# Performance work log

Hardware: AMD Instinct MI355X
Metric: run time of the kernel (lower is better)

Reference implementation:

```python
import jax, jax.numpy as jnp
import numpy as np

D_MODEL = 2048
HEADS = 32
HEAD_DIM = 64   # D_MODEL // HEADS
STATE = 256
KCONV = 4
CHUNK = 64
EPS = 1e-5
CONV_DIM = D_MODEL + 2 * STATE          # 2560 (n_groups=1)
PROJ = D_MODEL + CONV_DIM + HEADS       # 4640 (z | xBC | dt)
BATCH, SEQ = 2, 2048


def rmsnorm(x, w, eps=EPS):
    return x * jax.lax.rsqrt(jnp.mean(x * x, axis=-1, keepdims=True) + eps) * w


def setup_inputs() -> dict:
    key = jax.random.key(0)
    ks = jax.random.split(key, 8)
    x = jax.random.normal(ks[0], (BATCH, SEQ, D_MODEL), jnp.float32)
    norm_w = jnp.ones((D_MODEL,), jnp.float32)
    w_in = jax.random.normal(ks[1], (D_MODEL, PROJ), jnp.float32) * 0.02
    conv_w = jax.random.normal(ks[2], (CONV_DIM, KCONV), jnp.float32) * 0.2
    conv_b = jnp.zeros((CONV_DIM,), jnp.float32)
    # HF-style dt init: softplus(dt_bias) uniform-log in [1e-3, 1e-1]
    dt0 = jnp.exp(jax.random.uniform(ks[3], (HEADS,)) * (np.log(0.1) - np.log(0.001)) + np.log(0.001))
    dt_bias = dt0 + jnp.log(-jnp.expm1(-dt0))
    A_log = jnp.log(jnp.arange(1, HEADS + 1, dtype=jnp.float32))
    D_skip = jnp.ones((HEADS,), jnp.float32)
    gnorm_w = jnp.ones((D_MODEL,), jnp.float32)
    w_out = jax.random.normal(ks[4], (D_MODEL, D_MODEL), jnp.float32) * 0.02
    wo_w = jax.random.normal(ks[5], (D_MODEL, D_MODEL), jnp.float32) * 0.02
    return {"x": x, "norm_w": norm_w, "w_in": w_in, "conv_w": conv_w, "conv_b": conv_b,
            "dt_bias": dt_bias, "A_log": A_log, "D_skip": D_skip, "gnorm_w": gnorm_w,
            "w_out": w_out, "wo_w": wo_w}


def reference(x, norm_w, w_in, conv_w, conv_b, dt_bias, A_log, D_skip, gnorm_w, w_out, wo_w):
    b, L, _ = x.shape
    nc = L // CHUNK
    # pre-RMSNorm
    xn = rmsnorm(x, norm_w)
    # in_proj and split: z | xBC | dt
    proj = xn @ w_in
    z = proj[..., :D_MODEL]
    xBC = proj[..., D_MODEL:D_MODEL + CONV_DIM]
    dt = proj[..., D_MODEL + CONV_DIM:]                      # [b,L,H]
    # causal depthwise conv1d (kernel 4) + SiLU
    xp = jnp.pad(xBC, ((0, 0), (KCONV - 1, 0), (0, 0)))
    conv = conv_b + sum(xp[:, k:k + L] * conv_w[:, k] for k in range(KCONV))
    conv = jax.nn.silu(conv)
    xs = conv[..., :D_MODEL].reshape(b, L, HEADS, HEAD_DIM)  # SSM input
    Bm = conv[..., D_MODEL:D_MODEL + STATE]                  # [b,L,N] (n_groups=1)
    Cm = conv[..., D_MODEL + STATE:]                         # [b,L,N]
    dt = jax.nn.softplus(dt + dt_bias)                       # [b,L,H], >0
    A = -jnp.exp(A_log)                                      # [H]
    # ---- Mamba2 chunked selective scan (chunk_size=64) ----
    def ck(a):
        return a.reshape(b, nc, CHUNK, *a.shape[2:])
    xs_c, dt_c, B_c, C_c = ck(xs), ck(dt), ck(Bm), ck(Cm)
    Adt = dt_c * A                                           # [b,c,l,h] (<=0)
    Acs = jnp.cumsum(Adt, axis=2)
    # intra-chunk (diagonal blocks)
    seg = Acs[:, :, :, None, :] - Acs[:, :, None, :, :]      # [b,c,l,s,h]
    idx = jnp.arange(CHUNK)
    mask = (idx[:, None] >= idx[None, :])[None, None, :, :, None]
    Lmat = jnp.where(mask, jnp.exp(seg), 0.0)                # [b,c,l,s,h]
    CB = jnp.einsum('bcln,bcsn->bcls', C_c, B_c)
    xt = xs_c * dt_c[..., None]                              # [b,c,l,h,p]
    Y_diag = jnp.einsum('bclsh,bcshp->bclhp', CB[..., None] * Lmat, xt)
    # chunk-final states
    decay_states = jnp.exp(Acs[:, :, -1:, :] - Acs)          # [b,c,l,h]
    states = jnp.einsum('bcln,bclh,bclhp->bchpn', B_c, decay_states, xt)
    # inter-chunk recurrence (scan over nc chunks only)
    chunk_decay = jnp.exp(Acs[:, :, -1, :])                  # [b,c,h]
    def step(S, inp):
        dec, st = inp
        return S * dec[:, :, None, None] + st, S
    S0 = jnp.zeros((b, HEADS, HEAD_DIM, STATE), x.dtype)
    _, prev = jax.lax.scan(step, S0, (jnp.moveaxis(chunk_decay, 1, 0), jnp.moveaxis(states, 1, 0)))
    prev = jnp.moveaxis(prev, 0, 1)                          # [b,c,h,p,n] state at chunk start
    Y_off = jnp.einsum('bcln,bchpn,bclh->bclhp', C_c, prev, jnp.exp(Acs))
    y = (Y_diag + Y_off).reshape(b, L, HEADS, HEAD_DIM) + D_skip[None, None, :, None] * xs
    y = y.reshape(b, L, D_MODEL)
    # gated RMSNorm, out_proj, then wo
    y = rmsnorm(y * jax.nn.silu(z), gnorm_w)
    return (y @ w_out) @ wo_w
```

## Files before the change

kernel.cpp:

```cpp
#include <hip/hip_runtime.h>
#include <math.h>

#define D_MODEL 2048
#define HEADS 32
#define HEAD_DIM 64
#define STATE 256
#define KCONV 4
#define CHUNK 64
#define NC 32
#define SEQL 2048
#define BATCHN 2
#define CONV_DIMN 2560
#define PROJ_DIM 4640
#define PROJB_W 4608
#define EPSF 1e-5f
#define BL (BATCHN * SEQL)

typedef __attribute__((ext_vector_type(8))) short short8;
typedef __attribute__((ext_vector_type(4))) short short4v;
typedef __attribute__((ext_vector_type(4))) float f32x4;

__device__ __forceinline__ short f2bf(float f) {
  unsigned u = __builtin_bit_cast(unsigned, f);
  u = (u + 0x7fffu + ((u >> 16) & 1u)) >> 16;
  return (short)u;
}
__device__ __forceinline__ float b2f(short s) {
  unsigned u = ((unsigned)(unsigned short)s) << 16;
  return __builtin_bit_cast(float, u);
}
__device__ __forceinline__ void gld16(const void* g, void* l) {
  __builtin_amdgcn_global_load_lds((const __attribute__((address_space(1))) unsigned int*)g,
                                   (__attribute__((address_space(3))) unsigned int*)l,
                                   16, 0, 0);
}

__global__ __launch_bounds__(256) void rmsnorm_bf16_k(const float* __restrict__ x,
                                                      const float* __restrict__ w,
                                                      short* __restrict__ out) {
  int row = blockIdx.x;
  int t = threadIdx.x;
  const float4* x4 = (const float4*)(x + (size_t)row * D_MODEL);
  float4 va = x4[2 * t], vb = x4[2 * t + 1];
  float ss = va.x * va.x + va.y * va.y + va.z * va.z + va.w * va.w +
             vb.x * vb.x + vb.y * vb.y + vb.z * vb.z + vb.w * vb.w;
  #pragma unroll
  for (int off = 32; off > 0; off >>= 1) ss += __shfl_down(ss, off);
  __shared__ float ws_[4];
  if ((t & 63) == 0) ws_[t >> 6] = ss;
  __syncthreads();
  float tot = ws_[0] + ws_[1] + ws_[2] + ws_[3];
  float scale = rsqrtf(tot / (float)D_MODEL + EPSF);
  const float4* w4 = (const float4*)w;
  float4 wa = w4[2 * t], wb = w4[2 * t + 1];
  short tmp[8];
  tmp[0] = f2bf(va.x * scale * wa.x); tmp[1] = f2bf(va.y * scale * wa.y);
  tmp[2] = f2bf(va.z * scale * wa.z); tmp[3] = f2bf(va.w * scale * wa.w);
  tmp[4] = f2bf(vb.x * scale * wb.x); tmp[5] = f2bf(vb.y * scale * wb.y);
  tmp[6] = f2bf(vb.z * scale * wb.z); tmp[7] = f2bf(vb.w * scale * wb.w);
  *(int4*)(out + (size_t)row * D_MODEL + t * 8) = *(int4*)tmp;
}

__global__ __launch_bounds__(256) void transpose_bf16_k(const float* __restrict__ W,
                                                        short* __restrict__ WT,
                                                        int K, int ncols, int stride) {
  __shared__ float tile[32][33];
  int bn = blockIdx.x * 32, bk = blockIdx.y * 32;
  int tx = threadIdx.x & 31, ty = threadIdx.x >> 5;
  #pragma unroll
  for (int i = 0; i < 32; i += 8) {
    int k = bk + ty + i, n = bn + tx;
    tile[ty + i][tx] = (n < ncols) ? W[(size_t)k * stride + n] : 0.f;
  }
  __syncthreads();
  #pragma unroll
  for (int i = 0; i < 32; i += 8) {
    int n = bn + ty + i, k = bk + tx;
    WT[(size_t)n * K + k] = f2bf(tile[tx][ty + i]);
  }
}

__global__ __launch_bounds__(256) void dt_gemm_k(const float* __restrict__ x,
                                                 const float* __restrict__ norm_w,
                                                 const float* __restrict__ w_in,
                                                 float* __restrict__ dtraw) {
  int row = blockIdx.x;
  int t = threadIdx.x;
  __shared__ float sx[D_MODEL];
  __shared__ float red[8][32];
  __shared__ float sred[4];
  const float4* x4 = (const float4*)(x + (size_t)row * D_MODEL);
  const float4* nw4 = (const float4*)norm_w;
  float ss = 0.f;
  for (int i = t; i < D_MODEL / 4; i += 256) {
    float4 v = x4[i];
    ss += v.x * v.x + v.y * v.y + v.z * v.z + v.w * v.w;
    float4 nw = nw4[i];
    float4 pv; pv.x = v.x * nw.x; pv.y = v.y * nw.y; pv.z = v.z * nw.z; pv.w = v.w * nw.w;
    ((float4*)sx)[i] = pv;
  }
  #pragma unroll
  for (int off = 32; off > 0; off >>= 1) ss += __shfl_down(ss, off);
  if ((t & 63) == 0) sred[t >> 6] = ss;
  __syncthreads();
  float tot = sred[0] + sred[1] + sred[2] + sred[3];
  float scale = rsqrtf(tot / (float)D_MODEL + EPSF);
  int h = t & 31, sl = t >> 5;
  float acc = 0.f;
  for (int k = sl * 256; k < sl * 256 + 256; k++)
    acc += sx[k] * w_in[(size_t)k * PROJ_DIM + (D_MODEL + CONV_DIMN) + h];
  red[sl][h] = acc;
  __syncthreads();
  if (t < 32) {
    float s = 0.f;
    #pragma unroll
    for (int i = 0; i < 8; i++) s += red[i][t];
    dtraw[(size_t)row * HEADS + t] = s * scale;
  }
}

template<bool BF16OUT>
__global__ __launch_bounds__(256) void gemm_bt_k(const short* __restrict__ A,
                                                 const short* __restrict__ BT,
                                                 void* __restrict__ Cout,
                                                 int M, int N, int K) {
  __shared__ short sA[4096];
  __shared__ short sB[4096];
  int t = threadIdx.x;
  int lane = t & 63, w = t >> 6;
  int m0 = blockIdx.y * 128, n0 = blockIdx.x * 128;
  f32x4 acc[4][4] = {};
  int rS[2], ksS[2];
  #pragma unroll
  for (int ld = 0; ld < 2; ld++) {
    int c = w + ld * 4;
    int r = c * 16 + (lane >> 2);
    rS[ld] = r;
    ksS[ld] = (((lane & 3) ^ ((r >> 1) & 3))) * 8;
  }
  int q = lane >> 4, mr = lane & 15;
  int wm = (w & 1) * 64, wn = (w >> 1) * 64;
  int aoff[4], boff[4];
  #pragma unroll
  for (int i = 0; i < 4; i++) {
    int r = wm + i * 16 + mr;
    aoff[i] = r * 32 + (q ^ ((r >> 1) & 3)) * 8;
    int rn = wn + i * 16 + mr;
    boff[i] = rn * 32 + (q ^ ((rn >> 1) & 3)) * 8;
  }
  for (int k0 = 0; k0 < K; k0 += 32) {
    __syncthreads();
    #pragma unroll
    for (int ld = 0; ld < 2; ld++) {
      int c = w + ld * 4;
      gld16(A + (size_t)(m0 + rS[ld]) * K + k0 + ksS[ld], &sA[c * 512]);
      gld16(BT + (size_t)(n0 + rS[ld]) * K + k0 + ksS[ld], &sB[c * 512]);
    }
    __syncthreads();
    short8 af[4], bfr[4];
    #pragma unroll
    for (int i = 0; i < 4; i++) af[i] = *(const short8*)&sA[aoff[i]];
    #pragma unroll
    for (int i = 0; i < 4; i++) bfr[i] = *(const short8*)&sB[boff[i]];
    #pragma unroll
    for (int mi = 0; mi < 4; mi++)
      #pragma unroll
      for (int ni = 0; ni < 4; ni++)
        acc[mi][ni] = __builtin_amdgcn_mfma_f32_16x16x32_bf16(af[mi], bfr[ni], acc[mi][ni], 0, 0, 0);
  }
  int orow = (lane >> 4) * 4, ocol = lane & 15;
  #pragma unroll
  for (int mi = 0; mi < 4; mi++) {
    #pragma unroll
    for (int ni = 0; ni < 4; ni++) {
      int gn = n0 + wn + ni * 16 + ocol;
      if (gn >= N) continue;
      #pragma unroll
      for (int r = 0; r < 4; r++) {
        int gm = m0 + wm + mi * 16 + orow + r;
        if (BF16OUT) ((short*)Cout)[(size_t)gm * N + gn] = f2bf(acc[mi][ni][r]);
        else         ((float*)Cout)[(size_t)gm * N + gn] = acc[mi][ni][r];
      }
    }
  }
}

__global__ __launch_bounds__(256) void conv_silu_k(const short* __restrict__ projb,
                                                   const float* __restrict__ cw,
                                                   const float* __restrict__ cb,
                                                   short* __restrict__ out) {
  int idx = blockIdx.x * 256 + threadIdx.x;
  int c = idx % CONV_DIMN;
  int bt = idx / CONV_DIMN;
  int t = bt % SEQL;
  int b = bt / SEQL;
  float acc = cb[c];
  #pragma unroll
  for (int k = 0; k < KCONV; k++) {
    int tt = t - (KCONV - 1) + k;
    if (tt >= 0)
      acc += b2f(projb[((size_t)(b * SEQL + tt)) * PROJB_W + D_MODEL + c]) * cw[c * KCONV + k];
  }
  out[idx] = f2bf(acc / (1.f + expf(-acc)));
}

__global__ void dt_acs_k(const float* __restrict__ dtraw,
                         const float* __restrict__ dt_bias,
                         const float* __restrict__ A_log,
                         float* __restrict__ dtb, float* __restrict__ acsb) {
  int bc = blockIdx.x;
  int b = bc / NC, c = bc % NC;
  int l = threadIdx.x;
  int tok = c * CHUNK + l;
  size_t base = ((size_t)(b * SEQL + tok)) * HEADS;
  for (int h = 0; h < HEADS; h++) {
    float raw = dtraw[base + h] + dt_bias[h];
    float dt = raw > 20.f ? raw : log1pf(expf(raw));
    float adt = -expf(A_log[h]) * dt;
    float cs = adt;
    #pragma unroll
    for (int off = 1; off < 64; off <<= 1) {
      float v = __shfl_up(cs, off);
      if (l >= off) cs += v;
    }
    dtb[base + h] = dt;
    acsb[base + h] = cs;
  }
}

__global__ __launch_bounds__(256) void cb_k(const short* __restrict__ convb,
                                            short* __restrict__ CB) {
  int bc = blockIdx.x;
  int b = bc / NC, c = bc % NC;
  __shared__ float sC[64][65];
  __shared__ float sB[64][65];
  int t = threadIdx.x;
  int s = t & 63;
  int lb = (t >> 6) * 16;
  float acc[16] = {};
  size_t rowb = ((size_t)(b * SEQL + c * CHUNK)) * CONV_DIMN;
  for (int nt = 0; nt < 4; nt++) {
    __syncthreads();
    #pragma unroll
    for (int i = 0; i < 16; i++) {
      int e = t + 256 * i;
      int r = e >> 6, col = e & 63;
      sC[r][col] = b2f(convb[rowb + (size_t)r * CONV_DIMN + (D_MODEL + STATE) + nt * 64 + col]);
      sB[r][col] = b2f(convb[rowb + (size_t)r * CONV_DIMN + D_MODEL + nt * 64 + col]);
    }
    __syncthreads();
    for (int n = 0; n < 64; n++) {
      float bv = sB[s][n];
      #pragma unroll
      for (int j = 0; j < 16; j++) acc[j] += sC[lb + j][n] * bv;
    }
  }
  size_t ob = ((size_t)bc) * 64 * 64;
  #pragma unroll
  for (int j = 0; j < 16; j++) CB[ob + (size_t)(lb + j) * 64 + s] = f2bf(acc[j]);
}

__global__ __launch_bounds__(256) void chunk_states_k(const short* __restrict__ convb,
                                                      const float* __restrict__ dtb,
                                                      const float* __restrict__ acsb,
                                                      int b, short* __restrict__ G) {
  int blk = blockIdx.x;
  int h = blk & 31, c = blk >> 5;
  __shared__ __align__(16) short sXT[64][72];
  __shared__ __align__(16) short sBT[256][72];
  __shared__ float swt[64];
  int t = threadIdx.x;
  size_t rowb = ((size_t)(b * SEQL + c * CHUNK)) * CONV_DIMN;
  size_t ab = ((size_t)(b * SEQL + c * CHUNK)) * HEADS;
  if (t < 64) {
    float a = acsb[ab + (size_t)t * HEADS + h];
    float alast = acsb[ab + (size_t)63 * HEADS + h];
    swt[t] = expf(alast - a) * dtb[ab + (size_t)t * HEADS + h];
  }
  __syncthreads();
  #pragma unroll
  for (int i = 0; i < 4; i++) {
    int e = t + 256 * i;
    int l = e >> 4, p4 = (e & 15) * 4;
    short4v v = *(const short4v*)&convb[rowb + (size_t)l * CONV_DIMN + h * HEAD_DIM + p4];
    float wt = swt[l];
    short vv[4] = {v.x, v.y, v.z, v.w};
    #pragma unroll
    for (int j = 0; j < 4; j++) {
      int p = p4 + j;
      sXT[p][((((l >> 3) ^ ((p >> 2) & 7)) << 3) | (l & 7))] = f2bf(b2f(vv[j]) * wt);
    }
  }
  #pragma unroll
  for (int i = 0; i < 16; i++) {
    int e = t + 256 * i;
    int l = e >> 6, n4 = (e & 63) * 4;
    short4v v = *(const short4v*)&convb[rowb + (size_t)l * CONV_DIMN + D_MODEL + n4];
    short vv[4] = {v.x, v.y, v.z, v.w};
    #pragma unroll
    for (int j = 0; j < 4; j++) {
      int n = n4 + j;
      sBT[n][((((l >> 3) ^ ((n >> 2) & 7)) << 3) | (l & 7))] = vv[j];
    }
  }
  __syncthreads();
  int lane = t & 63, w = t >> 6;
  int mr = lane & 15, q = lane >> 4;
  f32x4 acc[4][4] = {};
  #pragma unroll
  for (int ks = 0; ks < 2; ks++) {
    short8 af[4], bfr[4];
    #pragma unroll
    for (int mi = 0; mi < 4; mi++) {
      int p = mi * 16 + mr;
      af[mi] = *(const short8*)&sXT[p][(((ks * 4 + q) ^ ((p >> 2) & 7)) << 3)];
    }
    #pragma unroll
    for (int ni = 0; ni < 4; ni++) {
      int n = w * 64 + ni * 16 + mr;
      bfr[ni] = *(const short8*)&sBT[n][(((ks * 4 + q) ^ ((n >> 2) & 7)) << 3)];
    }
    #pragma unroll
    for (int mi = 0; mi < 4; mi++)
      #pragma unroll
      for (int ni = 0; ni < 4; ni++)
        acc[mi][ni] = __builtin_amdgcn_mfma_f32_16x16x32_bf16(af[mi], bfr[ni], acc[mi][ni], 0, 0, 0);
  }
  size_t gb = (size_t)blk * (64 * 256);
  #pragma unroll
  for (int mi = 0; mi < 4; mi++)
    #pragma unroll
    for (int ni = 0; ni < 4; ni++)
      #pragma unroll
      for (int r = 0; r < 4; r++)
        G[gb + (size_t)(mi * 16 + q * 4 + r) * 256 + w * 64 + ni * 16 + mr] = f2bf(acc[mi][ni][r]);
}

__global__ __launch_bounds__(256) void scan_states_k(short* __restrict__ G,
                                                     const float* __restrict__ acsb,
                                                     int b) {
  int gid = blockIdx.x * 256 + threadIdx.x;
  int np = gid & 127;
  int p  = (gid >> 7) & 63;
  int h  = gid >> 13;
  float S0 = 0.f, S1 = 0.f;
  for (int c = 0; c < NC; c++) {
    size_t base = (((size_t)(c * HEADS + h) * 64) + p) * 256 + np * 2;
    unsigned u = *(const unsigned*)&G[base];
    float g0 = b2f((short)(u & 0xffff));
    float g1 = b2f((short)(u >> 16));
    unsigned wv = (unsigned)(unsigned short)f2bf(S0) | ((unsigned)(unsigned short)f2bf(S1) << 16);
    *(unsigned*)&G[base] = wv;
    float dec = expf(acsb[((size_t)(b * SEQL + c * CHUNK + 63)) * HEADS + h]);
    S0 = S0 * dec + g0;
    S1 = S1 * dec + g1;
  }
}

__global__ __launch_bounds__(256) void y_fused_k(const short* __restrict__ convb,
                                                 const short* __restrict__ CBb,
                                                 const short* __restrict__ G,
                                                 const float* __restrict__ dtb,
                                                 const float* __restrict__ acsb,
                                                 const float* __restrict__ D_skip,
                                                 int b, float* __restrict__ Y) {
  int blk = blockIdx.x;
  int h = blk & 31, c = blk >> 5;
  __shared__ __align__(16) short sM[64][72];
  __shared__ __align__(16) short sXT[64][72];
  __shared__ float sacs[64], sdt[64], sea[64];
  int t = threadIdx.x;
  int lane = t & 63, w = t >> 6;
  size_t rowb = ((size_t)(b * SEQL + c * CHUNK)) * CONV_DIMN;
  size_t ab = ((size_t)(b * SEQL + c * CHUNK)) * HEADS;
  size_t cbbase = ((size_t)(b * NC + c)) * 64 * 64;
  if (t < 64) {
    float a = acsb[ab + (size_t)t * HEADS + h];
    sacs[t] = a;
    sea[t] = expf(a);
    sdt[t] = dtb[ab + (size_t)t * HEADS + h];
  }
  __syncthreads();
  #pragma unroll
  for (int i = 0; i < 16; i++) {
    int e = t + 256 * i;
    int r = e >> 6, col = e & 63;
    float m = 0.f;
    if (col <= r)
      m = b2f(CBb[cbbase + (size_t)r * 64 + col]) * expf(sacs[r] - sacs[col]) * sdt[col];
    sM[r][col] = f2bf(m);
  }
  #pragma unroll
  for (int i = 0; i < 4; i++) {
    int e = t + 256 * i;
    int l = e >> 4, p4 = (e & 15) * 4;
    short4v v = *(const short4v*)&convb[rowb + (size_t)l * CONV_DIMN + h * HEAD_DIM + p4];
    short vv[4] = {v.x, v.y, v.z, v.w};
    #pragma unroll
    for (int j = 0; j < 4; j++) {
      int p = p4 + j;
      sXT[p][((((l >> 3) ^ ((p >> 2) & 7)) << 3) | (l & 7))] = vv[j];
    }
  }
  __syncthreads();
  int mr = lane & 15, q = lane >> 4;
  int wm = (w & 1) * 32, wn = (w >> 1) * 32;
  f32x4 acc1[2][2] = {}, acc2[2][2] = {};
  #pragma unroll
  for (int ks = 0; ks < 2; ks++) {
    short8 af[2], bfr[2];
    #pragma unroll
    for (int mi = 0; mi < 2; mi++)
      af[mi] = *(const short8*)&sM[wm + mi * 16 + mr][ks * 32 + q * 8];
    #pragma unroll
    for (int ni = 0; ni < 2; ni++) {
      int p = wn + ni * 16 + mr;
      bfr[ni] = *(const short8*)&sXT[p][(((ks * 4 + q) ^ ((p >> 2) & 7)) << 3)];
    }
    #pragma unroll
    for (int mi = 0; mi < 2; mi++)
      #pragma unroll
      for (int ni = 0; ni < 2; ni++)
        acc1[mi][ni] = __builtin_amdgcn_mfma_f32_16x16x32_bf16(af[mi], bfr[ni], acc1[mi][ni], 0, 0, 0);
  }
  const short* Crow = convb + rowb + (D_MODEL + STATE);
  size_t gbase = (size_t)blk * (64 * 256);
  #pragma unroll
  for (int st = 0; st < 8; st++) {
    short8 af[2], bfr[2];
    #pragma unroll
    for (int mi = 0; mi < 2; mi++) {
      int l = wm + mi * 16 + mr;
      af[mi] = *(const short8*)&Crow[(size_t)l * CONV_DIMN + st * 32 + q * 8];
    }
    #pragma unroll
    for (int ni = 0; ni < 2; ni++) {
      int p = wn + ni * 16 + mr;
      bfr[ni] = *(const short8*)&G[gbase + (size_t)p * 256 + st * 32 + q * 8];
    }
    #pragma unroll
    for (int mi = 0; mi < 2; mi++)
      #pragma unroll
      for (int ni = 0; ni < 2; ni++)
        acc2[mi][ni] = __builtin_amdgcn_mfma_f32_16x16x32_bf16(af[mi], bfr[ni], acc2[mi][ni], 0, 0, 0);
  }
  float dsk = D_skip[h];
  size_t ybase = ((size_t)(b * SEQL + c * CHUNK)) * D_MODEL + h * HEAD_DIM;
  #pragma unroll
  for (int mi = 0; mi < 2; mi++)
    #pragma unroll
    for (int ni = 0; ni < 2; ni++) {
      int p = wn + ni * 16 + mr;
      #pragma unroll
      for (int r = 0; r < 4; r++) {
        int l = wm + mi * 16 + q * 4 + r;
        float xsv = b2f(sXT[p][((((l >> 3) ^ ((p >> 2) & 7)) << 3) | (l & 7))]);
        Y[ybase + (size_t)l * D_MODEL + p] =
            acc1[mi][ni][r] + sea[l] * acc2[mi][ni][r] + dsk * xsv;
      }
    }
}

__global__ __launch_bounds__(256) void gated_norm_bf16_k(const float* __restrict__ Y,
                                                         const short* __restrict__ projb,
                                                         const float* __restrict__ gw,
                                                         short* __restrict__ out) {
  int row = blockIdx.x;
  int t = threadIdx.x;
  const float4* y4 = (const float4*)(Y + (size_t)row * D_MODEL);
  float4 ya = y4[2 * t], yb = y4[2 * t + 1];
  short zt[8];
  *(int4*)zt = *(const int4*)(projb + (size_t)row * PROJB_W + t * 8);
  float g[8];
  float yv[8] = {ya.x, ya.y, ya.z, ya.w, yb.x, yb.y, yb.z, yb.w};
  float ss = 0.f;
  #pragma unroll
  for (int i = 0; i < 8; i++) {
    float z = b2f(zt[i]);
    g[i] = yv[i] * (z / (1.f + expf(-z)));
    ss += g[i] * g[i];
  }
  #pragma unroll
  for (int off = 32; off > 0; off >>= 1) ss += __shfl_down(ss, off);
  __shared__ float ws_[4];
  if ((t & 63) == 0) ws_[t >> 6] = ss;
  __syncthreads();
  float tot = ws_[0] + ws_[1] + ws_[2] + ws_[3];
  float scale = rsqrtf(tot / (float)D_MODEL + EPSF);
  const float4* g4 = (const float4*)gw;
  float4 wa = g4[2 * t], wb = g4[2 * t + 1];
  float wv[8] = {wa.x, wa.y, wa.z, wa.w, wb.x, wb.y, wb.z, wb.w};
  short tmp[8];
  #pragma unroll
  for (int i = 0; i < 8; i++) tmp[i] = f2bf(g[i] * scale * wv[i]);
  *(int4*)(out + (size_t)row * D_MODEL + t * 8) = *(int4*)tmp;
}

extern "C" void kernel_launch(void* const* d_in, const int* in_sizes, int n_in,
                              void* d_out, int out_size, void* d_ws, size_t ws_size,
                              hipStream_t stream) {
  const float* x       = (const float*)d_in[0];
  const float* norm_w  = (const float*)d_in[1];
  const float* w_in    = (const float*)d_in[2];
  const float* conv_w  = (const float*)d_in[3];
  const float* conv_b  = (const float*)d_in[4];
  const float* dt_bias = (const float*)d_in[5];
  const float* A_log   = (const float*)d_in[6];
  const float* D_skip  = (const float*)d_in[7];
  const float* gnorm_w = (const float*)d_in[8];
  const float* w_out   = (const float*)d_in[9];
  const float* wo_w    = (const float*)d_in[10];
  float* out = (float*)d_out;

  float* ws    = (float*)d_ws;
  short* xnb   = (short*)ws;
  short* w_inT = (short*)(ws + 4194304);
  short* projb = (short*)(ws + 8912896);
  short* convb = (short*)(ws + 18350080);
  float* dtraw = ws + 23592960;
  float* dtb   = ws + 23724032;
  float* acsb  = ws + 23855104;
  short* CBb   = (short*)(ws + 23986176);
  float* Yb    = ws + 24117248;
  short* w_outT= (short*)(ws + 32505856);
  short* wo_wT = (short*)(ws + 34603008);
  short* G     = (short*)ws;
  short* Yg    = convb;
  short* t1b   = (short*)ws;

  rmsnorm_bf16_k<<<BL, 256, 0, stream>>>(x, norm_w, xnb);
  transpose_bf16_k<<<dim3(PROJB_W / 32, D_MODEL / 32), 256, 0, stream>>>(w_in, w_inT, D_MODEL, PROJB_W, PROJ_DIM);
  transpose_bf16_k<<<dim3(D_MODEL / 32, D_MODEL / 32), 256, 0, stream>>>(w_out, w_outT, D_MODEL, D_MODEL, D_MODEL);
  transpose_bf16_k<<<dim3(D_MODEL / 32, D_MODEL / 32), 256, 0, stream>>>(wo_w, wo_wT, D_MODEL, D_MODEL, D_MODEL);
  dt_gemm_k<<<BL, 256, 0, stream>>>(x, norm_w, w_in, dtraw);
  gemm_bt_k<true><<<dim3(PROJB_W / 128, BL / 128), 256, 0, stream>>>(xnb, w_inT, projb, BL, PROJB_W, D_MODEL);
  conv_silu_k<<<(BL * CONV_DIMN) / 256, 256, 0, stream>>>(projb, conv_w, conv_b, convb);
  dt_acs_k<<<BATCHN * NC, 64, 0, stream>>>(dtraw, dt_bias, A_log, dtb, acsb);
  cb_k<<<BATCHN * NC, 256, 0, stream>>>(convb, CBb);
  for (int b = 0; b < BATCHN; b++) {
    chunk_states_k<<<NC * HEADS, 256, 0, stream>>>(convb, dtb, acsb, b, G);
    scan_states_k<<<1024, 256, 0, stream>>>(G, acsb, b);
    y_fused_k<<<NC * HEADS, 256, 0, stream>>>(convb, CBb, G, dtb, acsb, D_skip, b, Yb);
  }
  gated_norm_bf16_k<<<BL, 256, 0, stream>>>(Yb, projb, gnorm_w, Yg);
  gemm_bt_k<true><<<dim3(D_MODEL / 128, BL / 128), 256, 0, stream>>>(Yg, w_outT, t1b, BL, D_MODEL, D_MODEL);
  gemm_bt_k<false><<<dim3(D_MODEL / 128, BL / 128), 256, 0, stream>>>(t1b, wo_wT, out, BL, D_MODEL, D_MODEL);
}
```

Measured before the change: 694.8 us.

## Replace GEMM with 256-wide tiles, 4-stage LDS pipeline and XCD block swizzle

Swaps the 128x128 single-buffered bf16 MFMA GEMM for a 512-thread kernel with 256x256 or 128x256 tiles and a 4-deep LDS ring buffer. Global loads are issued three tiles ahead and gated by explicit vmcnt waits, replacing the two barriers per k-step. Block IDs are swizzled across the 8 XCDs, and s_setprio is raised around the MFMA bursts. The aim is to hide global load latency and raise MFMA utilisation for the three projection GEMMs. The cost is much higher register and LDS use per block, plus fewer blocks for the square GEMMs.

```diff
diff --git a/kernel.cpp b/kernel.cpp
--- a/kernel.cpp
+++ b/kernel.cpp
@@ -119,70 +119,107 @@
   }
 }
 
-template<bool BF16OUT>
-__global__ __launch_bounds__(256) void gemm_bt_k(const short* __restrict__ A,
-                                                 const short* __restrict__ BT,
-                                                 void* __restrict__ Cout,
-                                                 int M, int N, int K) {
-  __shared__ short sA[4096];
-  __shared__ short sB[4096];
-  int t = threadIdx.x;
-  int lane = t & 63, w = t >> 6;
-  int m0 = blockIdx.y * 128, n0 = blockIdx.x * 128;
-  f32x4 acc[4][4] = {};
-  int rS[2], ksS[2];
-  #pragma unroll
-  for (int ld = 0; ld < 2; ld++) {
-    int c = w + ld * 4;
-    int r = c * 16 + (lane >> 2);
-    rS[ld] = r;
-    ksS[ld] = (((lane & 3) ^ ((r >> 1) & 3))) * 8;
-  }
-  int q = lane >> 4, mr = lane & 15;
-  int wm = (w & 1) * 64, wn = (w >> 1) * 64;
-  int aoff[4], boff[4];
-  #pragma unroll
-  for (int i = 0; i < 4; i++) {
-    int r = wm + i * 16 + mr;
-    aoff[i] = r * 32 + (q ^ ((r >> 1) & 3)) * 8;
-    int rn = wn + i * 16 + mr;
-    boff[i] = rn * 32 + (q ^ ((rn >> 1) & 3)) * 8;
-  }
-  for (int k0 = 0; k0 < K; k0 += 32) {
-    __syncthreads();
-    #pragma unroll
-    for (int ld = 0; ld < 2; ld++) {
-      int c = w + ld * 4;
-      gld16(A + (size_t)(m0 + rS[ld]) * K + k0 + ksS[ld], &sA[c * 512]);
-      gld16(BT + (size_t)(n0 + rS[ld]) * K + k0 + ksS[ld], &sB[c * 512]);
-    }
-    __syncthreads();
-    short8 af[4], bfr[4];
-    #pragma unroll
-    for (int i = 0; i < 4; i++) af[i] = *(const short8*)&sA[aoff[i]];
-    #pragma unroll
-    for (int i = 0; i < 4; i++) bfr[i] = *(const short8*)&sB[boff[i]];
+template<int BM, bool BF16OUT>
+__global__ __launch_bounds__(512, 2) void gemm256_k(const short* __restrict__ A,
+                                                    const short* __restrict__ BT,
+                                                    void* __restrict__ Cout,
+                                                    int M, int N, int K) {
+  constexpr int WM = BM / 128;
+  constexpr int WN = 8 / WM;
+  constexpr int NPW = 256 / WN;
+  constexpr int NF = NPW / 16;
+  constexpr int ABUF = BM * 32;
+  constexpr int BUFS = ABUF + 8192;
+  constexpr int ACALLS = BM / 128;
+  constexpr int LPT = ACALLS + 2;
+  __shared__ short lds[4 * BUFS];
+
+  const int t = threadIdx.x;
+  const int lane = t & 63, w = t >> 6;
+  const int mr = lane & 15, q = lane >> 4;
+  const int cq8 = (q ^ ((mr >> 1) & 3)) * 8;
+  const int stj = ((lane & 3) ^ ((lane >> 3) & 3)) * 8;
+  const int str = lane >> 2;
+
+  const int nbx = N >> 8;
+  const int nwg = nbx * (M / BM);
+  const int cpx = nwg >> 3;
+  const int bid = blockIdx.x;
+  const int swz = (bid & 7) * cpx + (bid >> 3);
+  const int bx = swz % nbx, by = swz / nbx;
+  const int m0 = by * BM, n0 = bx * 256;
+  const int wm = w % WM;
+  const int wn = w / WM;
+
+  const int NT = K >> 5;
+  f32x4 acc[8][NF] = {};
+
+  auto STAGE = [&](int tile) {
+    const int buf = tile & 3;
+    short* dst = &lds[buf * BUFS];
+    const int kb = tile * 32 + stj;
+    #pragma unroll
+    for (int cc = 0; cc < ACALLS; cc++) {
+      const int rr = w * (BM / 8) + cc * 16 + str;
+      gld16(A + (size_t)(m0 + rr) * K + kb, dst + (w * (BM / 8) + cc * 16) * 32);
+    }
+    const short* gB = BT + (size_t)(n0 + w * 32 + str) * K + kb;
+    short* dB = dst + ABUF + w * 1024;
+    gld16(gB, dB);
+    gld16(gB + (size_t)16 * K, dB + 512);
+  };
+
+  STAGE(0); STAGE(1); STAGE(2);
+  asm volatile("s_waitcnt vmcnt(%0)" :: "n"(2 * LPT) : "memory");
+  __builtin_amdgcn_s_barrier();
+
+  for (int tt = 0; tt < NT; ++tt) {
+    const short* sA = &lds[(tt & 3) * BUFS];
+    const short* sB = sA + ABUF;
+    if (tt + 3 < NT) STAGE(tt + 3);
+    short8 af[4], bfr[NF];
+    #pragma unroll
+    for (int ni = 0; ni < NF; ni++)
+      bfr[ni] = *(const short8*)&sB[(wn * NPW + ni * 16 + mr) * 32 + cq8];
     #pragma unroll
     for (int mi = 0; mi < 4; mi++)
-      #pragma unroll
-      for (int ni = 0; ni < 4; ni++)
+      af[mi] = *(const short8*)&sA[(wm * 128 + mi * 16 + mr) * 32 + cq8];
+    __builtin_amdgcn_s_setprio(1);
+    #pragma unroll
+    for (int mi = 0; mi < 4; mi++)
+      #pragma unroll
+      for (int ni = 0; ni < NF; ni++)
         acc[mi][ni] = __builtin_amdgcn_mfma_f32_16x16x32_bf16(af[mi], bfr[ni], acc[mi][ni], 0, 0, 0);
-  }
-  int orow = (lane >> 4) * 4, ocol = lane & 15;
-  #pragma unroll
-  for (int mi = 0; mi < 4; mi++) {
-    #pragma unroll
-    for (int ni = 0; ni < 4; ni++) {
-      int gn = n0 + wn + ni * 16 + ocol;
-      if (gn >= N) continue;
+    __builtin_amdgcn_s_setprio(0);
+    #pragma unroll
+    for (int mi = 0; mi < 4; mi++)
+      af[mi] = *(const short8*)&sA[(wm * 128 + 64 + mi * 16 + mr) * 32 + cq8];
+    __builtin_amdgcn_s_setprio(1);
+    #pragma unroll
+    for (int mi = 0; mi < 4; mi++)
+      #pragma unroll
+      for (int ni = 0; ni < NF; ni++)
+        acc[4 + mi][ni] = __builtin_amdgcn_mfma_f32_16x16x32_bf16(af[mi], bfr[ni], acc[4 + mi][ni], 0, 0, 0);
+    __builtin_amdgcn_s_setprio(0);
+    __builtin_amdgcn_sched_barrier(0);
+    if (tt + 3 < NT)      asm volatile("s_waitcnt vmcnt(%0)" :: "n"(2 * LPT) : "memory");
+    else if (tt + 2 < NT) asm volatile("s_waitcnt vmcnt(%0)" :: "n"(LPT) : "memory");
+    else                  asm volatile("s_waitcnt vmcnt(0)" ::: "memory");
+    __builtin_amdgcn_s_barrier();
+  }
+
+  #pragma unroll
+  for (int mi = 0; mi < 8; mi++)
+    #pragma unroll
+    for (int ni = 0; ni < NF; ni++) {
+      const int gm = m0 + wm * 128 + mi * 16 + q * 4;
+      const int gn = n0 + wn * NPW + ni * 16 + mr;
       #pragma unroll
       for (int r = 0; r < 4; r++) {
-        int gm = m0 + wm + mi * 16 + orow + r;
-        if (BF16OUT) ((short*)Cout)[(size_t)gm * N + gn] = f2bf(acc[mi][ni][r]);
-        else         ((float*)Cout)[(size_t)gm * N + gn] = acc[mi][ni][r];
+        if (BF16OUT) ((short*)Cout)[(size_t)(gm + r) * N + gn] = f2bf(acc[mi][ni][r]);
+        else         ((float*)Cout)[(size_t)(gm + r) * N + gn] = acc[mi][ni][r];
       }
     }
-  }
 }
 
 __global__ __launch_bounds__(256) void conv_silu_k(const short* __restrict__ projb,
@@ -533,7 +570,7 @@
   transpose_bf16_k<<<dim3(D_MODEL / 32, D_MODEL / 32), 256, 0, stream>>>(w_out, w_outT, D_MODEL, D_MODEL, D_MODEL);
   transpose_bf16_k<<<dim3(D_MODEL / 32, D_MODEL / 32), 256, 0, stream>>>(wo_w, wo_wT, D_MODEL, D_MODEL, D_MODEL);
   dt_gemm_k<<<BL, 256, 0, stream>>>(x, norm_w, w_in, dtraw);
-  gemm_bt_k<true><<<dim3(PROJB_W / 128, BL / 128), 256, 0, stream>>>(xnb, w_inT, projb, BL, PROJB_W, D_MODEL);
+  gemm256_k<256, true><<<(BL / 256) * (PROJB_W / 256), 512, 0, stream>>>(xnb, w_inT, projb, BL, PROJB_W, D_MODEL);
   conv_silu_k<<<(BL * CONV_DIMN) / 256, 256, 0, stream>>>(projb, conv_w, conv_b, convb);
   dt_acs_k<<<BATCHN * NC, 64, 0, stream>>>(dtraw, dt_bias, A_log, dtb, acsb);
   cb_k<<<BATCHN * NC, 256, 0, stream>>>(convb, CBb);
@@ -543,6 +580,6 @@
     y_fused_k<<<NC * HEADS, 256, 0, stream>>>(convb, CBb, G, dtb, acsb, D_skip, b, Yb);
   }
   gated_norm_bf16_k<<<BL, 256, 0, stream>>>(Yb, projb, gnorm_w, Yg);
-  gemm_bt_k<true><<<dim3(D_MODEL / 128, BL / 128), 256, 0, stream>>>(Yg, w_outT, t1b, BL, D_MODEL, D_MODEL);
-  gemm_bt_k<false><<<dim3(D_MODEL / 128, BL / 128), 256, 0, stream>>>(t1b, wo_wT, out, BL, D_MODEL, D_MODEL);
-}
+  gemm256_k<128, true><<<(BL / 128) * (D_MODEL / 256), 512, 0, stream>>>(Yg, w_outT, t1b, BL, D_MODEL, D_MODEL);
+  gemm256_k<128, false><<<(BL / 128) * (D_MODEL / 256), 512, 0, stream>>>(t1b, wo_wT, out, BL, D_MODEL, D_MODEL);
+}
```

Result: faster. 673.7 us (-3.0%).
